# Kernel tuning notes

Hardware: AMD Instinct MI355X
Metric: run time of the kernel (lower is better)

Reference implementation:

```python
import jax, jax.numpy as jnp
import numpy as np

H = 1024      # hidden_size
I = 4096      # intermediate_size
E = 8         # num_experts
TOP_K = 2
LB_COEF = 0.01


def setup_inputs() -> dict:
    key = jax.random.key(0)
    ks = jax.random.split(key, 8)
    s_h = 1.0 / np.sqrt(H)
    s_i = 1.0 / np.sqrt(I)
    return {
        "x": jax.random.normal(ks[0], (2, 2048, H), dtype=jnp.float32),
        "Wr": jax.random.normal(ks[1], (H, E), dtype=jnp.float32) * s_h,
        "br": jnp.zeros((E,), dtype=jnp.float32),
        "W1": jax.random.normal(ks[2], (E, H, I), dtype=jnp.float32) * s_h,
        "b1": jnp.zeros((E, I), dtype=jnp.float32),
        "W2": jax.random.normal(ks[3], (E, I, H), dtype=jnp.float32) * s_i,
        "b2": jnp.zeros((E, H), dtype=jnp.float32),
    }


def _moe_forward(x, Wr, br, W1, b1, W2, b2):
    B, S, Hd = x.shape
    x_flat = x.reshape(-1, Hd)                      # [T, H]
    T = x_flat.shape[0]

    # ---- Router: softmax probs, top-k, renormalize ----
    logits = x_flat @ Wr + br                       # [T, E]
    probs = jax.nn.softmax(logits, axis=-1)         # [T, E]
    topk_w, topk_idx = jax.lax.top_k(probs, TOP_K)  # [T, K]
    topk_w = topk_w / jnp.sum(topk_w, axis=-1, keepdims=True)

    # ---- Load-balance aux loss (switch-style) ----
    onehot = jax.nn.one_hot(topk_idx, E, dtype=x.dtype)   # [T, K, E]
    frac_tokens = onehot.mean(axis=(0, 1))                 # [E]
    frac_probs = probs.mean(axis=0)                        # [E]
    aux_loss = E * jnp.sum(frac_tokens * frac_probs) * LB_COEF

    # combine_weights[t, e] = routing weight of expert e for token t (0 if unselected)
    combine = jnp.sum(topk_w[..., None] * onehot, axis=1)  # [T, E]

    # ---- Experts: dense per-expert FFN, weighted combine ----
    out = jnp.zeros_like(x_flat)
    for e in range(E):
        h = jax.nn.gelu(x_flat @ W1[e] + b1[e])            # [T, I]
        y = h @ W2[e] + b2[e]                              # [T, H]
        out = out + y * combine[:, e:e + 1]
    return out.reshape(B, S, Hd), aux_loss


def reference(x, Wr, br, W1, b1, W2, b2):
    return _moe_forward(x, Wr, br, W1, b1, W2, b2)
```

## Files before the change

### kernel.cpp

```cpp
#include <hip/hip_runtime.h>
#include <hip/hip_bf16.h>

#define HD 1024
#define ID 4096
#define NE 8
#define NT 4096
#define NSLOT (NT*2)

typedef __attribute__((ext_vector_type(4))) float f32x4;
typedef __attribute__((ext_vector_type(8))) short bf16x8;
typedef __attribute__((ext_vector_type(4))) unsigned int u32x4;
typedef __attribute__((ext_vector_type(2))) unsigned int u32x2;
typedef unsigned short u16;

__device__ __forceinline__ u16 f2b(float f) {
  __hip_bfloat16 h = __float2bfloat16(f);
  return __builtin_bit_cast(unsigned short, h);
}
__device__ __forceinline__ unsigned int pack2(float a, float b) {
  return (unsigned int)f2b(a) | ((unsigned int)f2b(b) << 16);
}
__device__ __forceinline__ void gload16(const void* g, void* l) {
  __builtin_amdgcn_global_load_lds(
      (const __attribute__((address_space(1))) unsigned int*)g,
      (__attribute__((address_space(3))) unsigned int*)l, 16, 0, 0);
}
__device__ __forceinline__ float gelu_tanh(float v) {
  float c = v + 0.044715f * v * v * v;
  return 0.5f * v * (1.0f + tanhf(0.7978845608028654f * c));
}

__global__ void k_convert_x(const float* __restrict__ x, u16* __restrict__ xb) {
  int i = blockIdx.x * 256 + threadIdx.x;
  const f32x4* x4 = (const f32x4*)x;
  f32x4 a = x4[2 * i], b = x4[2 * i + 1];
  u32x4 r;
  r[0] = pack2(a[0], a[1]); r[1] = pack2(a[2], a[3]);
  r[2] = pack2(b[0], b[1]); r[3] = pack2(b[2], b[3]);
  ((u32x4*)xb)[i] = r;
}

__global__ __launch_bounds__(256) void k_transpose_bf16(
    const float* __restrict__ src, u16* __restrict__ dst, int R, int C) {
  __shared__ float tile[64][65];
  int e = blockIdx.z;
  int c0 = blockIdx.x * 64;
  int r0 = blockIdx.y * 64;
  int t = threadIdx.x;
  const float* s = src + (size_t)e * R * C;
#pragma unroll
  for (int i = 0; i < 16; ++i) {
    int r = i * 4 + (t >> 6);
    tile[r][t & 63] = s[(size_t)(r0 + r) * C + c0 + (t & 63)];
  }
  __syncthreads();
  u16* d = dst + (size_t)e * R * C;
#pragma unroll
  for (int i = 0; i < 4; ++i) {
    int c = i * 16 + (t >> 4);
    int rb = (t & 15) * 4;
    u32x2 p;
    p[0] = pack2(tile[rb + 0][c], tile[rb + 1][c]);
    p[1] = pack2(tile[rb + 2][c], tile[rb + 3][c]);
    *(u32x2*)&d[(size_t)(c0 + c) * R + r0 + rb] = p;
  }
}

__global__ __launch_bounds__(256) void k_router(
    const float* __restrict__ x, const float* __restrict__ Wr,
    const float* __restrict__ br, int* __restrict__ cnt,
    int* __restrict__ slotE, int* __restrict__ slotLoc,
    float* __restrict__ slotW, float* __restrict__ probsAll) {
  __shared__ float wrt[NE * HD];
  int t = threadIdx.x;
  for (int i = t; i < NE * HD; i += 256) wrt[(i & 7) * HD + (i >> 3)] = Wr[i];
  __syncthreads();
  int wave = t >> 6, lane = t & 63;
  int token = blockIdx.x * 4 + wave;
  const float* xr = x + (size_t)token * HD;
  float acc[NE] = {0, 0, 0, 0, 0, 0, 0, 0};
#pragma unroll 4
  for (int j = 0; j < 16; ++j) {
    int h = j * 64 + lane;
    float xv = xr[h];
#pragma unroll
    for (int e = 0; e < NE; ++e) acc[e] += xv * wrt[e * HD + h];
  }
#pragma unroll
  for (int d = 1; d < 64; d <<= 1) {
#pragma unroll
    for (int e = 0; e < NE; ++e) acc[e] += __shfl_xor(acc[e], d, 64);
  }
  if (lane == 0) {
    float lg[NE], p[NE];
    float m = -1e30f;
#pragma unroll
    for (int e = 0; e < NE; ++e) { lg[e] = acc[e] + br[e]; m = fmaxf(m, lg[e]); }
    float s = 0.f;
#pragma unroll
    for (int e = 0; e < NE; ++e) { p[e] = expf(lg[e] - m); s += p[e]; }
    float inv = 1.0f / s;
    int i1 = 0, i2 = -1;
    float v1 = -1.f, v2 = -1.f;
#pragma unroll
    for (int e = 0; e < NE; ++e) {
      p[e] *= inv;
      probsAll[token * NE + e] = p[e];
      if (p[e] > v1) { v2 = v1; i2 = i1; v1 = p[e]; i1 = e; }
      else if (p[e] > v2) { v2 = p[e]; i2 = e; }
    }
    float wsum = v1 + v2;
    int l1 = atomicAdd(&cnt[i1], 1);
    int l2 = atomicAdd(&cnt[i2], 1);
    slotE[token * 2] = i1;     slotLoc[token * 2] = l1;     slotW[token * 2] = v1 / wsum;
    slotE[token * 2 + 1] = i2; slotLoc[token * 2 + 1] = l2; slotW[token * 2 + 1] = v2 / wsum;
  }
}

__global__ __launch_bounds__(256) void k_psum(const float* __restrict__ probsAll,
                                              float* __restrict__ psumG) {
  __shared__ float red[256];
  int t = threadIdx.x;
  int base = blockIdx.x * 128;
  float s = 0.f;
  for (int i = t >> 3; i < 128; i += 32) s += probsAll[(base + i) * NE + (t & 7)];
  red[t] = s;
  __syncthreads();
  for (int st = 128; st >= 8; st >>= 1) {
    if (t < st) red[t] += red[t + st];
    __syncthreads();
  }
  if (t < 8) atomicAdd(&psumG[t], red[t]);
}

__global__ void k_finalize(const float* __restrict__ psumG, const int* __restrict__ cnt,
                           int* __restrict__ off, float* __restrict__ out_aux) {
  if (threadIdx.x == 0) {
    int o = 0;
    float a = 0.f;
    for (int e = 0; e < NE; ++e) {
      off[e] = o;
      o += cnt[e];
      a += ((float)cnt[e] / (float)NSLOT) * (psumG[e] / (float)NT);
    }
    off[NE] = o;
    out_aux[0] = (float)NE * a * 0.01f;
  }
}

__global__ void k_scatter(const int* __restrict__ slotE, const int* __restrict__ slotLoc,
                          const float* __restrict__ slotW, const int* __restrict__ off,
                          int* __restrict__ rowTok, float* __restrict__ rowW) {
  int i = blockIdx.x * 256 + threadIdx.x;
  int pos = off[slotE[i]] + slotLoc[i];
  if (pos < 0) pos = 0;
  if (pos >= NSLOT) pos = NSLOT - 1;
  rowTok[pos] = i >> 1;
  rowW[pos] = slotW[i];
}

#define STG(bf) do { \
    gload16(srcA0, &As[bf][c0 * 8]); \
    gload16(srcA1, &As[bf][c1 * 8]); \
    gload16(srcB0, &Bs[bf][c0 * 8]); \
    gload16(srcB1, &Bs[bf][c1 * 8]); \
    srcA0 += 32; srcA1 += 32; srcB0 += 32; srcB1 += 32; \
  } while (0)

__global__ __launch_bounds__(256, 3) void k_gemm1(
    const u16* __restrict__ xb, const u16* __restrict__ w1t,
    const float* __restrict__ b1, u16* __restrict__ hbuf,
    const int* __restrict__ cnt, const int* __restrict__ off,
    const int* __restrict__ rowTok) {
  const int NWG = NE * 32 * 32;
  int bid = blockIdx.x;
  int wg = (bid & 7) * (NWG / 8) + (bid >> 3);
  int e = wg >> 10;
  int rem = wg & 1023;
  int m0 = (rem >> 5) * 128;
  int n0 = (rem & 31) * 128;
  int ce = cnt[e];
  if (m0 >= ce) return;
  int oe = off[e];
  __shared__ u16 As[2][128 * 32];
  __shared__ u16 Bs[2][128 * 32];
  __shared__ int rtok[128];
  int t = threadIdx.x;
  if (t < 128) {
    int r = m0 + t;
    if (r >= ce) r = ce - 1;
    int tok = rowTok[oe + r];
    rtok[t] = (tok < 0) ? 0 : (tok >= NT ? NT - 1 : tok);
  }
  __syncthreads();
  int c0 = t, c1 = t + 256;
  int js0 = (c0 & 3) ^ ((c0 >> 3) & 3);
  int js1 = (c1 & 3) ^ ((c1 >> 3) & 3);
  const u16* srcA0 = xb + (size_t)rtok[c0 >> 2] * HD + js0 * 8;
  const u16* srcA1 = xb + (size_t)rtok[c1 >> 2] * HD + js1 * 8;
  const u16* bb = w1t + (size_t)e * ID * HD + (size_t)n0 * HD;
  const u16* srcB0 = bb + (size_t)(c0 >> 2) * HD + js0 * 8;
  const u16* srcB1 = bb + (size_t)(c1 >> 2) * HD + js1 * 8;
  int wave = t >> 6, lane = t & 63;
  int wr = wave >> 1, wc = wave & 1;
  int arow = wr * 64 + (lane & 15);
  int aoff = arow * 32 + ((lane >> 4) ^ ((arow >> 1) & 3)) * 8;
  int brow = wc * 64 + (lane & 15);
  int boff = brow * 32 + ((lane >> 4) ^ ((brow >> 1) & 3)) * 8;
  f32x4 acc[4][4] = {};
  const int NK = HD / 32;
  STG(0);
  STG(1);
#pragma unroll 2
  for (int kt = 0; kt < NK; ++kt) {
    if (kt + 1 < NK) asm volatile("s_waitcnt vmcnt(4)" ::: "memory");
    else             asm volatile("s_waitcnt vmcnt(0)" ::: "memory");
    __builtin_amdgcn_s_barrier();
    int cb = kt & 1;
    const u16* ap = &As[cb][aoff];
    const u16* bp = &Bs[cb][boff];
    bf16x8 af[4], bfr[4];
#pragma unroll
    for (int m = 0; m < 4; ++m) af[m] = *(const bf16x8*)(ap + m * 16 * 32);
#pragma unroll
    for (int n = 0; n < 4; ++n) bfr[n] = *(const bf16x8*)(bp + n * 16 * 32);
#pragma unroll
    for (int m = 0; m < 4; ++m)
#pragma unroll
      for (int n = 0; n < 4; ++n)
        acc[m][n] = __builtin_amdgcn_mfma_f32_16x16x32_bf16(af[m], bfr[n], acc[m][n], 0, 0, 0);
    if (kt + 2 < NK) {
      __builtin_amdgcn_s_barrier();
      STG(cb);
    }
  }
  const float* b1e = b1 + (size_t)e * ID + n0;
#pragma unroll
  for (int n = 0; n < 4; ++n) {
    int col = wc * 64 + n * 16 + (lane & 15);
    float bias = b1e[col];
#pragma unroll
    for (int m = 0; m < 4; ++m) {
      int rbase = wr * 64 + m * 16 + (lane >> 4) * 4;
#pragma unroll
      for (int r = 0; r < 4; ++r) {
        int grow = m0 + rbase + r;
        if (grow < ce) {
          float v = acc[m][n][r] + bias;
          hbuf[(size_t)(oe + grow) * ID + n0 + col] = f2b(gelu_tanh(v));
        }
      }
    }
  }
}

__global__ __launch_bounds__(256, 3) void k_gemm2(
    const u16* __restrict__ hbuf, const u16* __restrict__ w2t,
    const float* __restrict__ b2, float* __restrict__ out,
    const int* __restrict__ cnt, const int* __restrict__ off,
    const int* __restrict__ rowTok, const float* __restrict__ rowW) {
  const int NWG = NE * 32 * 2 * 8;
  int bid = blockIdx.x;
  int wg = (bid & 7) * (NWG / 8) + (bid >> 3);
  int e = wg >> 9;
  int rem = wg & 511;
  int m0 = (rem >> 4) * 128;
  int ks = (rem >> 3) & 1;
  int n0 = (rem & 7) * 128;
  int ce = cnt[e];
  if (m0 >= ce) return;
  int oe = off[e];
  int k0 = ks * (ID / 2);
  __shared__ u16 As[2][128 * 32];
  __shared__ u16 Bs[2][128 * 32];
  __shared__ int rtok[128];
  __shared__ float rw[128];
  int t = threadIdx.x;
  if (t < 128) {
    int r = m0 + t;
    int rc = (r < ce) ? r : ce - 1;
    int tok = rowTok[oe + rc];
    rtok[t] = (tok < 0) ? 0 : (tok >= NT ? NT - 1 : tok);
    rw[t] = (r < ce) ? rowW[oe + r] : 0.0f;
  }
  __syncthreads();
  int c0 = t, c1 = t + 256;
  int js0 = (c0 & 3) ^ ((c0 >> 3) & 3);
  int js1 = (c1 & 3) ^ ((c1 >> 3) & 3);
  int rA0 = m0 + (c0 >> 2); if (rA0 >= ce) rA0 = ce - 1;
  int rA1 = m0 + (c1 >> 2); if (rA1 >= ce) rA1 = ce - 1;
  const u16* srcA0 = hbuf + (size_t)(oe + rA0) * ID + k0 + js0 * 8;
  const u16* srcA1 = hbuf + (size_t)(oe + rA1) * ID + k0 + js1 * 8;
  const u16* bb = w2t + (size_t)e * HD * ID + (size_t)n0 * ID + k0;
  const u16* srcB0 = bb + (size_t)(c0 >> 2) * ID + js0 * 8;
  const u16* srcB1 = bb + (size_t)(c1 >> 2) * ID + js1 * 8;
  int wave = t >> 6, lane = t & 63;
  int wr = wave >> 1, wc = wave & 1;
  int arow = wr * 64 + (lane & 15);
  int aoff = arow * 32 + ((lane >> 4) ^ ((arow >> 1) & 3)) * 8;
  int brow = wc * 64 + (lane & 15);
  int boff = brow * 32 + ((lane >> 4) ^ ((brow >> 1) & 3)) * 8;
  f32x4 acc[4][4] = {};
  const int NK = (ID / 2) / 32;
  STG(0);
  STG(1);
#pragma unroll 2
  for (int kt = 0; kt < NK; ++kt) {
    if (kt + 1 < NK) asm volatile("s_waitcnt vmcnt(4)" ::: "memory");
    else             asm volatile("s_waitcnt vmcnt(0)" ::: "memory");
    __builtin_amdgcn_s_barrier();
    int cb = kt & 1;
    const u16* ap = &As[cb][aoff];
    const u16* bp = &Bs[cb][boff];
    bf16x8 af[4], bfr[4];
#pragma unroll
    for (int m = 0; m < 4; ++m) af[m] = *(const bf16x8*)(ap + m * 16 * 32);
#pragma unroll
    for (int n = 0; n < 4; ++n) bfr[n] = *(const bf16x8*)(bp + n * 16 * 32);
#pragma unroll
    for (int m = 0; m < 4; ++m)
#pragma unroll
      for (int n = 0; n < 4; ++n)
        acc[m][n] = __builtin_amdgcn_mfma_f32_16x16x32_bf16(af[m], bfr[n], acc[m][n], 0, 0, 0);
    if (kt + 2 < NK) {
      __builtin_amdgcn_s_barrier();
      STG(cb);
    }
  }
  const float* b2e = b2 + (size_t)e * HD + n0;
#pragma unroll
  for (int n = 0; n < 4; ++n) {
    int col = wc * 64 + n * 16 + (lane & 15);
    float bias = (ks == 0) ? b2e[col] : 0.0f;
#pragma unroll
    for (int m = 0; m < 4; ++m) {
      int rbase = wr * 64 + m * 16 + (lane >> 4) * 4;
#pragma unroll
      for (int r = 0; r < 4; ++r) {
        int grow = m0 + rbase + r;
        if (grow < ce) {
          float v = (acc[m][n][r] + bias) * rw[rbase + r];
          atomicAdd(&out[(size_t)rtok[rbase + r] * HD + n0 + col], v);
        }
      }
    }
  }
}

extern "C" void kernel_launch(void* const* d_in, const int* in_sizes, int n_in,
                              void* d_out, int out_size, void* d_ws, size_t ws_size,
                              hipStream_t stream) {
  const float* x  = (const float*)d_in[0];
  const float* Wr = (const float*)d_in[1];
  const float* br = (const float*)d_in[2];
  const float* W1 = (const float*)d_in[3];
  const float* b1 = (const float*)d_in[4];
  const float* W2 = (const float*)d_in[5];
  const float* b2 = (const float*)d_in[6];
  float* out = (float*)d_out;

  char* ws = (char*)d_ws;
  size_t o = 0;
  auto alloc = [&](size_t bytes) {
    void* p = ws + o;
    o = (o + bytes + 255) & ~(size_t)255;
    return p;
  };
  u16* xb    = (u16*)alloc((size_t)NT * HD * 2);
  u16* w1t   = (u16*)alloc((size_t)NE * ID * HD * 2);
  u16* w2t   = (u16*)alloc((size_t)NE * ID * HD * 2);
  u16* hbuf  = (u16*)alloc((size_t)NSLOT * ID * 2);
  int* cnt     = (int*)alloc(NE * 4);
  float* psumG = (float*)alloc(NE * 4);
  int* off     = (int*)alloc(16 * 4);
  int* slotE   = (int*)alloc(NSLOT * 4);
  int* slotLoc = (int*)alloc(NSLOT * 4);
  float* slotW = (float*)alloc(NSLOT * 4);
  int* rowTok  = (int*)alloc(NSLOT * 4);
  float* rowW  = (float*)alloc(NSLOT * 4);
  float* probsAll = (float*)alloc((size_t)NT * NE * 4);

  if (ws_size < o) return;

  hipMemsetAsync(cnt, 0, NE * 4, stream);
  hipMemsetAsync(psumG, 0, NE * 4, stream);
  hipMemsetAsync(out, 0, (size_t)out_size * 4, stream);
  k_convert_x<<<(NT * HD / 8) / 256, 256, 0, stream>>>(x, xb);
  k_transpose_bf16<<<dim3(ID / 64, HD / 64, NE), 256, 0, stream>>>(W1, w1t, HD, ID);
  k_transpose_bf16<<<dim3(HD / 64, ID / 64, NE), 256, 0, stream>>>(W2, w2t, ID, HD);
  k_router<<<NT / 4, 256, 0, stream>>>(x, Wr, br, cnt, slotE, slotLoc, slotW, probsAll);
  k_psum<<<32, 256, 0, stream>>>(probsAll, psumG);
  k_finalize<<<1, 64, 0, stream>>>(psumG, cnt, off, out + (size_t)NT * HD);
  k_scatter<<<NSLOT / 256, 256, 0, stream>>>(slotE, slotLoc, slotW, off, rowTok, rowW);
  k_gemm1<<<NE * 32 * 32, 256, 0, stream>>>(xb, w1t, b1, hbuf, cnt, off, rowTok);
  k_gemm2<<<NE * 32 * 2 * 8, 256, 0, stream>>>(hbuf, w2t, b2, out, cnt, off, rowTok, rowW);
}
```

Baseline: 518.6 us.

## Enlarge grouped GEMM tiles to 256x256x64 with 512-thread workgroups

Both expert GEMMs move from 128x128 tiles with K-step 32 and 256 threads to 256x256 tiles with K-step 64 and 512 threads (8 waves, each computing 128x64). The LDS swizzle is widened to 8 slots. The XCD-aware block remapping is dropped. The larger tiles raise arithmetic intensity and cut global reloads of weights and activations, at the cost of more LDS (128KB double-buffered) and registers, occupancy of one block per CU, and coarser padding waste on ragged per-expert row counts.

Result: slower. 581.7 us (+12.2%).

```diff
diff --git a/kernel.cpp b/kernel.cpp
--- a/kernel.cpp
+++ b/kernel.cpp
@@ -160,93 +160,99 @@
 }
 
 #define STG(bf) do { \
-    gload16(srcA0, &As[bf][c0 * 8]); \
-    gload16(srcA1, &As[bf][c1 * 8]); \
-    gload16(srcB0, &Bs[bf][c0 * 8]); \
-    gload16(srcB1, &Bs[bf][c1 * 8]); \
-    srcA0 += 32; srcA1 += 32; srcB0 += 32; srcB1 += 32; \
+    _Pragma("unroll") \
+    for (int i_ = 0; i_ < 4; ++i_) { \
+      gload16(aSrc[i_], &As[bf][dstc[i_]]); \
+      gload16(bSrc[i_], &Bs[bf][dstc[i_]]); \
+      aSrc[i_] += 64; bSrc[i_] += 64; \
+    } \
   } while (0)
 
-__global__ __launch_bounds__(256, 3) void k_gemm1(
+__global__ __launch_bounds__(512, 1) void k_gemm1(
     const u16* __restrict__ xb, const u16* __restrict__ w1t,
     const float* __restrict__ b1, u16* __restrict__ hbuf,
     const int* __restrict__ cnt, const int* __restrict__ off,
     const int* __restrict__ rowTok) {
-  const int NWG = NE * 32 * 32;
   int bid = blockIdx.x;
-  int wg = (bid & 7) * (NWG / 8) + (bid >> 3);
-  int e = wg >> 10;
-  int rem = wg & 1023;
-  int m0 = (rem >> 5) * 128;
-  int n0 = (rem & 31) * 128;
+  int e = bid >> 8;
+  int m0 = ((bid >> 4) & 15) * 256;
+  int n0 = (bid & 15) * 256;
   int ce = cnt[e];
   if (m0 >= ce) return;
   int oe = off[e];
-  __shared__ u16 As[2][128 * 32];
-  __shared__ u16 Bs[2][128 * 32];
-  __shared__ int rtok[128];
+  __shared__ u16 As[2][256 * 64];
+  __shared__ u16 Bs[2][256 * 64];
+  __shared__ int rtok[256];
   int t = threadIdx.x;
-  if (t < 128) {
+  if (t < 256) {
     int r = m0 + t;
     if (r >= ce) r = ce - 1;
     int tok = rowTok[oe + r];
     rtok[t] = (tok < 0) ? 0 : (tok >= NT ? NT - 1 : tok);
   }
   __syncthreads();
-  int c0 = t, c1 = t + 256;
-  int js0 = (c0 & 3) ^ ((c0 >> 3) & 3);
-  int js1 = (c1 & 3) ^ ((c1 >> 3) & 3);
-  const u16* srcA0 = xb + (size_t)rtok[c0 >> 2] * HD + js0 * 8;
-  const u16* srcA1 = xb + (size_t)rtok[c1 >> 2] * HD + js1 * 8;
+  const u16* aSrc[4];
+  const u16* bSrc[4];
+  int dstc[4];
   const u16* bb = w1t + (size_t)e * ID * HD + (size_t)n0 * HD;
-  const u16* srcB0 = bb + (size_t)(c0 >> 2) * HD + js0 * 8;
-  const u16* srcB1 = bb + (size_t)(c1 >> 2) * HD + js1 * 8;
-  int wave = t >> 6, lane = t & 63;
-  int wr = wave >> 1, wc = wave & 1;
-  int arow = wr * 64 + (lane & 15);
-  int aoff = arow * 32 + ((lane >> 4) ^ ((arow >> 1) & 3)) * 8;
-  int brow = wc * 64 + (lane & 15);
-  int boff = brow * 32 + ((lane >> 4) ^ ((brow >> 1) & 3)) * 8;
-  f32x4 acc[4][4] = {};
-  const int NK = HD / 32;
+#pragma unroll
+  for (int i = 0; i < 4; ++i) {
+    int c = t + 512 * i;
+    int row = c >> 3, slot = c & 7, j = slot ^ (row & 7);
+    aSrc[i] = xb + (size_t)rtok[row] * HD + j * 8;
+    bSrc[i] = bb + (size_t)row * HD + j * 8;
+    dstc[i] = c * 8;
+  }
+  int lane = t & 63, wave = t >> 6;
+  int wr = wave >> 2, wc = wave & 3;
+  f32x4 acc[8][4] = {};
+  const int NK = HD / 64;
   STG(0);
   STG(1);
-#pragma unroll 2
   for (int kt = 0; kt < NK; ++kt) {
-    if (kt + 1 < NK) asm volatile("s_waitcnt vmcnt(4)" ::: "memory");
+    if (kt + 1 < NK) asm volatile("s_waitcnt vmcnt(8)" ::: "memory");
     else             asm volatile("s_waitcnt vmcnt(0)" ::: "memory");
     __builtin_amdgcn_s_barrier();
     int cb = kt & 1;
-    const u16* ap = &As[cb][aoff];
-    const u16* bp = &Bs[cb][boff];
-    bf16x8 af[4], bfr[4];
-#pragma unroll
-    for (int m = 0; m < 4; ++m) af[m] = *(const bf16x8*)(ap + m * 16 * 32);
-#pragma unroll
-    for (int n = 0; n < 4; ++n) bfr[n] = *(const bf16x8*)(bp + n * 16 * 32);
-#pragma unroll
-    for (int m = 0; m < 4; ++m)
-#pragma unroll
-      for (int n = 0; n < 4; ++n)
-        acc[m][n] = __builtin_amdgcn_mfma_f32_16x16x32_bf16(af[m], bfr[n], acc[m][n], 0, 0, 0);
+#pragma unroll
+    for (int kk = 0; kk < 2; ++kk) {
+      bf16x8 af[8], bv[4];
+#pragma unroll
+      for (int mm = 0; mm < 8; ++mm) {
+        int ra = wr * 128 + mm * 16 + (lane & 15);
+        int slot = (kk * 4 + (lane >> 4)) ^ (ra & 7);
+        af[mm] = *(const bf16x8*)&As[cb][ra * 64 + slot * 8];
+      }
+#pragma unroll
+      for (int nn = 0; nn < 4; ++nn) {
+        int rb = wc * 64 + nn * 16 + (lane & 15);
+        int slot = (kk * 4 + (lane >> 4)) ^ (rb & 7);
+        bv[nn] = *(const bf16x8*)&Bs[cb][rb * 64 + slot * 8];
+      }
+#pragma unroll
+      for (int mm = 0; mm < 8; ++mm)
+#pragma unroll
+        for (int nn = 0; nn < 4; ++nn)
+          acc[mm][nn] = __builtin_amdgcn_mfma_f32_16x16x32_bf16(af[mm], bv[nn], acc[mm][nn], 0, 0, 0);
+    }
     if (kt + 2 < NK) {
       __builtin_amdgcn_s_barrier();
-      STG(cb);
+      STG(kt & 1);
     }
   }
   const float* b1e = b1 + (size_t)e * ID + n0;
 #pragma unroll
-  for (int n = 0; n < 4; ++n) {
-    int col = wc * 64 + n * 16 + (lane & 15);
+  for (int nn = 0; nn < 4; ++nn) {
+    int col = wc * 64 + nn * 16 + (lane & 15);
     float bias = b1e[col];
 #pragma unroll
-    for (int m = 0; m < 4; ++m) {
-      int rbase = wr * 64 + m * 16 + (lane >> 4) * 4;
+    for (int mm = 0; mm < 8; ++mm) {
+      int lr0 = wr * 128 + mm * 16 + (lane >> 4) * 4;
 #pragma unroll
       for (int r = 0; r < 4; ++r) {
-        int grow = m0 + rbase + r;
+        int grow = m0 + lr0 + r;
         if (grow < ce) {
-          float v = acc[m][n][r] + bias;
+          float v = acc[mm][nn][r] + bias;
           hbuf[(size_t)(oe + grow) * ID + n0 + col] = f2b(gelu_tanh(v));
         }
       }
@@ -254,29 +260,26 @@
   }
 }
 
-__global__ __launch_bounds__(256, 3) void k_gemm2(
+__global__ __launch_bounds__(512, 1) void k_gemm2(
     const u16* __restrict__ hbuf, const u16* __restrict__ w2t,
     const float* __restrict__ b2, float* __restrict__ out,
     const int* __restrict__ cnt, const int* __restrict__ off,
     const int* __restrict__ rowTok, const float* __restrict__ rowW) {
-  const int NWG = NE * 32 * 2 * 8;
   int bid = blockIdx.x;
-  int wg = (bid & 7) * (NWG / 8) + (bid >> 3);
-  int e = wg >> 9;
-  int rem = wg & 511;
-  int m0 = (rem >> 4) * 128;
-  int ks = (rem >> 3) & 1;
-  int n0 = (rem & 7) * 128;
+  int e = bid >> 7;
+  int m0 = ((bid >> 3) & 15) * 256;
+  int n0 = ((bid >> 1) & 3) * 256;
+  int ks = bid & 1;
   int ce = cnt[e];
   if (m0 >= ce) return;
   int oe = off[e];
   int k0 = ks * (ID / 2);
-  __shared__ u16 As[2][128 * 32];
-  __shared__ u16 Bs[2][128 * 32];
-  __shared__ int rtok[128];
-  __shared__ float rw[128];
+  __shared__ u16 As[2][256 * 64];
+  __shared__ u16 Bs[2][256 * 64];
+  __shared__ int rtok[256];
+  __shared__ float rw[256];
   int t = threadIdx.x;
-  if (t < 128) {
+  if (t < 256) {
     int r = m0 + t;
     int rc = (r < ce) ? r : ce - 1;
     int tok = rowTok[oe + rc];
@@ -284,63 +287,71 @@
     rw[t] = (r < ce) ? rowW[oe + r] : 0.0f;
   }
   __syncthreads();
-  int c0 = t, c1 = t + 256;
-  int js0 = (c0 & 3) ^ ((c0 >> 3) & 3);
-  int js1 = (c1 & 3) ^ ((c1 >> 3) & 3);
-  int rA0 = m0 + (c0 >> 2); if (rA0 >= ce) rA0 = ce - 1;
-  int rA1 = m0 + (c1 >> 2); if (rA1 >= ce) rA1 = ce - 1;
-  const u16* srcA0 = hbuf + (size_t)(oe + rA0) * ID + k0 + js0 * 8;
-  const u16* srcA1 = hbuf + (size_t)(oe + rA1) * ID + k0 + js1 * 8;
+  const u16* aSrc[4];
+  const u16* bSrc[4];
+  int dstc[4];
   const u16* bb = w2t + (size_t)e * HD * ID + (size_t)n0 * ID + k0;
-  const u16* srcB0 = bb + (size_t)(c0 >> 2) * ID + js0 * 8;
-  const u16* srcB1 = bb + (size_t)(c1 >> 2) * ID + js1 * 8;
-  int wave = t >> 6, lane = t & 63;
-  int wr = wave >> 1, wc = wave & 1;
-  int arow = wr * 64 + (lane & 15);
-  int aoff = arow * 32 + ((lane >> 4) ^ ((arow >> 1) & 3)) * 8;
-  int brow = wc * 64 + (lane & 15);
-  int boff = brow * 32 + ((lane >> 4) ^ ((brow >> 1) & 3)) * 8;
-  f32x4 acc[4][4] = {};
-  const int NK = (ID / 2) / 32;
+#pragma unroll
+  for (int i = 0; i < 4; ++i) {
+    int c = t + 512 * i;
+    int row = c >> 3, slot = c & 7, j = slot ^ (row & 7);
+    int rA = m0 + row; if (rA >= ce) rA = ce - 1;
+    aSrc[i] = hbuf + (size_t)(oe + rA) * ID + k0 + j * 8;
+    bSrc[i] = bb + (size_t)row * ID + j * 8;
+    dstc[i] = c * 8;
+  }
+  int lane = t & 63, wave = t >> 6;
+  int wr = wave >> 2, wc = wave & 3;
+  f32x4 acc[8][4] = {};
+  const int NK = (ID / 2) / 64;
   STG(0);
   STG(1);
-#pragma unroll 2
   for (int kt = 0; kt < NK; ++kt) {
-    if (kt + 1 < NK) asm volatile("s_waitcnt vmcnt(4)" ::: "memory");
+    if (kt + 1 < NK) asm volatile("s_waitcnt vmcnt(8)" ::: "memory");
     else             asm volatile("s_waitcnt vmcnt(0)" ::: "memory");
     __builtin_amdgcn_s_barrier();
     int cb = kt & 1;
-    const u16* ap = &As[cb][aoff];
-    const u16* bp = &Bs[cb][boff];
-    bf16x8 af[4], bfr[4];
-#pragma unroll
-    for (int m = 0; m < 4; ++m) af[m] = *(const bf16x8*)(ap + m * 16 * 32);
-#pragma unroll
-    for (int n = 0; n < 4; ++n) bfr[n] = *(const bf16x8*)(bp + n * 16 * 32);
-#pragma unroll
-    for (int m = 0; m < 4; ++m)
-#pragma unroll
-      for (int n = 0; n < 4; ++n)
-        acc[m][n] = __builtin_amdgcn_mfma_f32_16x16x32_bf16(af[m], bfr[n], acc[m][n], 0, 0, 0);
+#pragma unroll
+    for (int kk = 0; kk < 2; ++kk) {
+      bf16x8 af[8], bv[4];
+#pragma unroll
+      for (int mm = 0; mm < 8; ++mm) {
+        int ra = wr * 128 + mm * 16 + (lane & 15);
+        int slot = (kk * 4 + (lane >> 4)) ^ (ra & 7);
+        af[mm] = *(const bf16x8*)&As[cb][ra * 64 + slot * 8];
+      }
+#pragma unroll
+      for (int nn = 0; nn < 4; ++nn) {
+        int rb = wc * 64 + nn * 16 + (lane & 15);
+        int slot = (kk * 4 + (lane >> 4)) ^ (rb & 7);
+        bv[nn] = *(const bf16x8*)&Bs[cb][rb * 64 + slot * 8];
+      }
+#pragma unroll
+      for (int mm = 0; mm < 8; ++mm)
+#pragma unroll
+        for (int nn = 0; nn < 4; ++nn)
+          acc[mm][nn] = __builtin_amdgcn_mfma_f32_16x16x32_bf16(af[mm], bv[nn], acc[mm][nn], 0, 0, 0);
+    }
     if (kt + 2 < NK) {
       __builtin_amdgcn_s_barrier();
-      STG(cb);
+      STG(kt & 1);
     }
   }
   const float* b2e = b2 + (size_t)e * HD + n0;
 #pragma unroll
-  for (int n = 0; n < 4; ++n) {
-    int col = wc * 64 + n * 16 + (lane & 15);
+  for (int nn = 0; nn < 4; ++nn) {
+    int col = wc * 64 + nn * 16 + (lane & 15);
     float bias = (ks == 0) ? b2e[col] : 0.0f;
 #pragma unroll
-    for (int m = 0; m < 4; ++m) {
-      int rbase = wr * 64 + m * 16 + (lane >> 4) * 4;
+    for (int mm = 0; mm < 8; ++mm) {
+      int lr0 = wr * 128 + mm * 16 + (lane >> 4) * 4;
 #pragma unroll
       for (int r = 0; r < 4; ++r) {
-        int grow = m0 + rbase + r;
+        int lr = lr0 + r;
+        int grow = m0 + lr;
         if (grow < ce) {
-          float v = (acc[m][n][r] + bias) * rw[rbase + r];
-          atomicAdd(&out[(size_t)rtok[rbase + r] * HD + n0 + col], v);
+          float v = (acc[mm][nn][r] + bias) * rw[lr];
+          atomicAdd(&out[(size_t)rtok[lr] * HD + n0 + col], v);
         }
       }
     }
@@ -392,6 +403,6 @@
   k_psum<<<32, 256, 0, stream>>>(probsAll, psumG);
   k_finalize<<<1, 64, 0, stream>>>(psumG, cnt, off, out + (size_t)NT * HD);
   k_scatter<<<NSLOT / 256, 256, 0, stream>>>(slotE, slotLoc, slotW, off, rowTok, rowW);
-  k_gemm1<<<NE * 32 * 32, 256, 0, stream>>>(xb, w1t, b1, hbuf, cnt, off, rowTok);
-  k_gemm2<<<NE * 32 * 2 * 8, 256, 0, stream>>>(hbuf, w2t, b2, out, cnt, off, rowTok, rowW);
-}
+  k_gemm1<<<NE * 16 * 16, 512, 0, stream>>>(xb, w1t, b1, hbuf, cnt, off, rowTok);
+  k_gemm2<<<NE * 16 * 4 * 2, 512, 0, stream>>>(hbuf, w2t, b2, out, cnt, off, rowTok, rowW);
+}
```
